# Kernel tuning notes

Hardware: AMD Instinct MI355X
Metric: run time of the kernel (lower is better)

The kernel has to match this reference:

```python
import jax, jax.numpy as jnp
import numpy as np

N = 100_000   # nodes
E = 1_600_000 # edges (avg degree 16)
D_IN = 128
D_H = 128
PROP_STEP = 2


def setup_inputs() -> dict:
    key = jax.random.key(0)
    k = jax.random.split(key, 6)
    in_feat = jax.random.normal(k[0], (N, D_IN), dtype=jnp.float32)
    edge_index = jax.random.randint(k[1], (2, E), 0, N, dtype=jnp.int64)
    s1 = 1.0 / np.sqrt(D_IN)
    s2 = 1.0 / np.sqrt(D_H)
    W1 = jax.random.normal(k[2], (D_IN, D_H), dtype=jnp.float32) * s1
    b1 = jnp.zeros((D_H,), dtype=jnp.float32)
    W2 = jax.random.normal(k[3], (D_H, D_H), dtype=jnp.float32) * s2
    b2 = jnp.zeros((D_H,), dtype=jnp.float32)
    return {"in_feat": in_feat, "edge_index": edge_index,
            "W1": W1, "b1": b1, "W2": W2, "b2": b2}


def _degree_norms(src, dst):
    ones = jnp.ones((src.shape[0],), dtype=jnp.float32)
    deg_out = jax.ops.segment_sum(ones, src, num_segments=N)
    deg_in = jax.ops.segment_sum(ones, dst, num_segments=N)
    # DGL clamps degree to >= 1 before norm='both'
    dout = jnp.maximum(deg_out, 1.0) ** -0.5  # applied to source features
    din = jnp.maximum(deg_in, 1.0) ** -0.5    # applied after aggregation
    return dout, din


def _gcn_conv(x, src, dst, dout, din, W, b):
    # D_in^{-1/2} A D_out^{-1/2} X W + b  (DGL GraphConv, norm='both')
    m = (x * dout[:, None])[src]                      # [E, D] gather
    agg = jax.ops.segment_sum(m, dst, num_segments=N) # [N, D] scatter-add
    return (agg * din[:, None]) @ W + b


def reference(in_feat, edge_index, W1, b1, W2, b2):
    src, dst = edge_index[0], edge_index[1]
    dout, din = _degree_norms(src, dst)
    h = _gcn_conv(in_feat, src, dst, dout, din, W1, b1)
    for _ in range(1, PROP_STEP):
        # relu=False and eval mode -> no relu / dropout
        h = _gcn_conv(h, src, dst, dout, din, W2, b2)
    return h
```

## Files before the change

### kernel.cpp

```cpp
#include <hip/hip_runtime.h>
#include <cstdint>
#include <cstddef>

#define DF 128
#define PB 512
#define RSH 8
#define RNG 256
#define CAP 6144

typedef short bf16x8 __attribute__((ext_vector_type(8)));
typedef float f32x4 __attribute__((ext_vector_type(4)));

__device__ __forceinline__ unsigned short f2b(float f) {
  unsigned u = __builtin_bit_cast(unsigned, f);
  u = (u + 0x7FFFu + ((u >> 16) & 1u)) >> 16;
  return (unsigned short)u;
}
__device__ __forceinline__ float b2f(unsigned short h) {
  return __builtin_bit_cast(float, (unsigned)h << 16);
}
__device__ __forceinline__ unsigned pack2(float lo, float hi) {
  return (unsigned)f2b(lo) | ((unsigned)f2b(hi) << 16);
}

__device__ __forceinline__ int edge_at(const void* ei, long long idx, int is32) {
  return is32 ? ((const int*)ei)[idx] : (int)((const long long*)ei)[idx];
}

__device__ __forceinline__ int detect_is32(const void* ei, long long lo, long long hi,
                                           int* s_flag) {
  int t = threadIdx.x;
  if (t == 0) *s_flag = 0;
  __syncthreads();
  int bad = 0;
  long long cap = lo + 2048; if (cap > hi) cap = hi;
  for (long long e = lo + t; e < cap; e += blockDim.x)
    bad |= (((const unsigned*)ei)[2 * e + 1] != 0);
  if (bad) atomicOr(s_flag, 1);
  __syncthreads();
  return *s_flag;
}

__global__ __launch_bounds__(256) void part_count_kernel(
    const void* __restrict__ ei, long long E, int nbuck, int chunk,
    int* __restrict__ H) {
  __shared__ int hd[512], hs[512], s_flag;
  int blk = blockIdx.x, t = threadIdx.x;
  for (int i = t; i < 512; i += 256) { hd[i] = 0; hs[i] = 0; }
  long long lo = (long long)blk * chunk;
  long long hi = lo + chunk; if (hi > E) hi = E;
  int is32 = detect_is32(ei, lo, hi, &s_flag);
  for (long long e = lo + t; e < hi; e += 256) {
    int s = edge_at(ei, e, is32);
    int d = edge_at(ei, E + e, is32);
    atomicAdd(&hs[s >> RSH], 1);
    atomicAdd(&hd[d >> RSH], 1);
  }
  __syncthreads();
  for (int b = t; b < nbuck; b += 256) {
    H[(size_t)b * PB + blk] = hd[b];
    H[((size_t)nbuck + b) * PB + blk] = hs[b];
  }
}

__device__ __forceinline__ int wave_incl_scan(int v, int lane) {
#pragma unroll
  for (int off = 1; off < 64; off <<= 1) {
    int t = __shfl_up(v, off, 64);
    if (lane >= off) v += t;
  }
  return v;
}

__global__ void chunk_sum_kernel(const int* __restrict__ deg, int* __restrict__ partials,
                                 int n, int nb,
                                 const float* __restrict__ W1, const float* __restrict__ W2,
                                 unsigned short* __restrict__ Wswz) {
  if ((int)blockIdx.x >= nb) {
    int chunk = ((int)blockIdx.x - nb) * 1024 + threadIdx.x;
    if (chunk < 8192) {
      int w = chunk >> 12;
      int rem = chunk & 4095;
      int part = rem >> 11;
      int tt = (rem >> 6) & 31;
      int l = rem & 63;
      int jb = tt >> 2, ks = tt & 3;
      const float* W = w ? W2 : W1;
      int c = jb * 16 + (l & 15);
      int k0 = ks * 32 + ((l >> 4) << 3);
      unsigned v[4];
#pragma unroll
      for (int p = 0; p < 4; ++p) {
        float f0 = W[(size_t)(k0 + 2 * p) * DF + c];
        float f1 = W[(size_t)(k0 + 2 * p + 1) * DF + c];
        unsigned short h0 = f2b(f0), h1 = f2b(f1);
        unsigned short o0 = part ? f2b(f0 - b2f(h0)) : h0;
        unsigned short o1 = part ? f2b(f1 - b2f(h1)) : h1;
        v[p] = (unsigned)o0 | ((unsigned)o1 << 16);
      }
      uint4 o; o.x = v[0]; o.y = v[1]; o.z = v[2]; o.w = v[3];
      ((uint4*)Wswz)[chunk] = o;
    }
    return;
  }
  __shared__ int wsum[16];
  int tid = threadIdx.x, lane = tid & 63, wid = tid >> 6;
  int base = blockIdx.x * 4096 + tid * 4;
  int s = 0;
#pragma unroll
  for (int q = 0; q < 4; ++q) { int i = base + q; if (i < n) s += deg[i]; }
#pragma unroll
  for (int off = 32; off; off >>= 1) s += __shfl_down(s, off, 64);
  if (lane == 0) wsum[wid] = s;
  __syncthreads();
  if (tid == 0) {
    int t = 0;
#pragma unroll
    for (int w = 0; w < 16; ++w) t += wsum[w];
    partials[blockIdx.x] = t;
  }
}

__global__ void scan_partials_kernel(int* __restrict__ partials, int nb) {
  int lane = threadIdx.x;
  int carry = 0;
  for (int base = 0; base < nb; base += 64) {
    int i = base + lane;
    int v = (i < nb) ? partials[i] : 0;
    int s = wave_incl_scan(v, lane);
    if (i < nb) partials[i] = s - v + carry;
    carry += __shfl(s, 63, 64);
  }
}

__global__ void scan_chunk_kernel(const int* __restrict__ deg, const int* __restrict__ chunk_off,
                                  int* __restrict__ row_ptr, int n) {
  __shared__ int wsum[16];
  int tid = threadIdx.x, lane = tid & 63, wid = tid >> 6;
  int base = blockIdx.x * 4096 + tid * 4;
  int v0 = (base + 0 < n) ? deg[base + 0] : 0;
  int v1 = (base + 1 < n) ? deg[base + 1] : 0;
  int v2 = (base + 2 < n) ? deg[base + 2] : 0;
  int v3 = (base + 3 < n) ? deg[base + 3] : 0;
  int p0 = v0, p1 = p0 + v1, p2 = p1 + v2, p3 = p2 + v3;
  int ws = wave_incl_scan(p3, lane);
  if (lane == 63) wsum[wid] = ws;
  __syncthreads();
  if (wid == 0) {
    int x = (lane < 16) ? wsum[lane] : 0;
    x = wave_incl_scan(x, lane);
    if (lane < 16) wsum[lane] = x;
  }
  __syncthreads();
  int off = (wid > 0 ? wsum[wid - 1] : 0) + (ws - p3) + chunk_off[blockIdx.x];
  if (base + 0 < n) row_ptr[base + 1] = off + p0;
  if (base + 1 < n) row_ptr[base + 2] = off + p1;
  if (base + 2 < n) row_ptr[base + 3] = off + p2;
  if (base + 3 < n) row_ptr[base + 4] = off + p3;
  if (blockIdx.x == 0 && tid == 0) row_ptr[0] = 0;
}

__global__ __launch_bounds__(256) void part_scatter_kernel(
    const void* __restrict__ ei, long long E, int nbuck, int chunk,
    const int* __restrict__ Hs, unsigned* __restrict__ pack_d,
    unsigned char* __restrict__ src_loc) {
  __shared__ int hd[512], hs[512], bd[512], bs[512];
  __shared__ int s_flag;
  int blk = blockIdx.x, t = threadIdx.x;
  for (int i = t; i < 512; i += 256) { hd[i] = 0; hs[i] = 0; }
  for (int b = t; b < nbuck; b += 256) {
    bd[b] = Hs[(size_t)b * PB + blk];
    bs[b] = Hs[((size_t)nbuck + b) * PB + blk] - (int)E;
  }
  long long lo = (long long)blk * chunk;
  long long hi = lo + chunk; if (hi > E) hi = E;
  int is32 = detect_is32(ei, lo, hi, &s_flag);
  for (long long e = lo + t; e < hi; e += 256) {
    int s = edge_at(ei, e, is32);
    int d = edge_at(ei, E + e, is32);
    int kb = d >> RSH;
    int rd = atomicAdd(&hd[kb], 1);
    pack_d[bd[kb] + rd] = ((unsigned)(d & (RNG - 1)) << 24) | (unsigned)s;
    int ks = s >> RSH;
    int rs = atomicAdd(&hs[ks], 1);
    src_loc[bs[ks] + rs] = (unsigned char)(s & (RNG - 1));
  }
}

__global__ __launch_bounds__(256) void bucket_build_kernel(
    const unsigned* __restrict__ pack_d, const unsigned char* __restrict__ src_loc,
    const int* __restrict__ Hs, int nbuck, long long E, int n,
    int* __restrict__ row_ptr, float* __restrict__ nin, float* __restrict__ nout,
    int* __restrict__ csr_src,
    const float* __restrict__ in_feat, unsigned short* __restrict__ x1h) {
  __shared__ unsigned stage[CAP];
  __shared__ int cnt[RNG], cur[RNG], woff[4];
  __shared__ float fn[RNG];
  int b = blockIdx.x, t = threadIdx.x;
  int lane = t & 63, wv = t >> 6;
  int start = Hs[(size_t)b * PB];
  int end = Hs[(size_t)(b + 1) * PB];
  int len = end - start;
  cnt[t] = 0;
  __syncthreads();
  bool fits = (len <= CAP);
  for (int i = t; i < len; i += 256) {
    unsigned p = pack_d[start + i];
    if (fits) stage[i] = p;
    atomicAdd(&cnt[p >> 24], 1);
  }
  __syncthreads();
  int dreg = cnt[t];
  int isc = wave_incl_scan(dreg, lane);
  if (lane == 63) woff[wv] = isc;
  __syncthreads();
  int add = 0;
#pragma unroll
  for (int w = 0; w < 4; ++w) if (w < wv) add += woff[w];
  int excl = isc - dreg + add;
  int nd = b * RNG + t;
  if (nd < n) {
    row_ptr[nd] = start + excl;
    nin[nd] = rsqrtf((float)(dreg > 1 ? dreg : 1));
  }
  if (b == (int)gridDim.x - 1 && t == 0) row_ptr[n] = (int)E;
  cur[t] = excl;
  __syncthreads();
  for (int i = t; i < len; i += 256) {
    unsigned p = fits ? stage[i] : pack_d[start + i];
    int dl = (int)(p >> 24);
    int r = atomicAdd(&cur[dl], 1);
    csr_src[start + r] = (int)(p & 0xFFFFFFu);
  }
  __syncthreads();
  cnt[t] = 0;
  __syncthreads();
  int sstart = Hs[(size_t)(nbuck + b) * PB] - (int)E;
  int send = Hs[(size_t)(nbuck + b + 1) * PB] - (int)E;
  for (int i = sstart + t; i < send; i += 256) atomicAdd(&cnt[src_loc[i]], 1);
  __syncthreads();
  float nv = rsqrtf((float)(cnt[t] > 1 ? cnt[t] : 1));
  fn[t] = nv;
  if (nd < n) nout[nd] = nv;
  __syncthreads();
  for (int c = t; c < RNG * DF / 8; c += 256) {
    int jl = c >> 4;
    int node = b * RNG + jl;
    if (node >= n) break;
    float s = fn[jl];
    long long base = (long long)node * DF + (c & 15) * 8;
    float4 a = *((const float4*)(in_feat + base));
    float4 bb = *((const float4*)(in_feat + base + 4));
    uint4 o;
    o.x = pack2(a.x * s, a.y * s);
    o.y = pack2(a.z * s, a.w * s);
    o.z = pack2(bb.x * s, bb.y * s);
    o.w = pack2(bb.z * s, bb.w * s);
    *((uint4*)(x1h + base)) = o;
  }
}

__global__ __launch_bounds__(256) void aggregate_bf16_kernel(
    const unsigned short* __restrict__ xh, const int* __restrict__ row_ptr,
    const int* __restrict__ csr_src, unsigned short* __restrict__ aggh, int n) {
  int wave = blockIdx.x * (blockDim.x >> 6) + (threadIdx.x >> 6);
  int lane = threadIdx.x & 63;
  if (wave >= n) return;
  int beg = row_ptr[wave], end = row_ptr[wave + 1];
  int deg = end - beg;
  int half = lane >> 5;
  int sub = lane & 31;
  float ax = 0.f, ay = 0.f, az = 0.f, aw = 0.f;
  for (int j0 = 0; j0 < deg; j0 += 64) {
    int li = beg + j0 + lane;
    int idx = csr_src[li < end ? li : (end - 1)];
    int cnt = deg - j0; if (cnt > 64) cnt = 64;
    int tfull = (cnt >> 4) << 3;
    for (int t0 = 0; t0 < tfull; t0 += 8) {
      ushort4 v[8];
#pragma unroll
      for (int u = 0; u < 8; ++u) {
        int s = __shfl(idx, 2 * (t0 + u) + half, 64);
        v[u] = *((const ushort4*)(xh + (size_t)s * DF) + sub);
      }
#pragma unroll
      for (int u = 0; u < 8; ++u) {
        ax += b2f(v[u].x); ay += b2f(v[u].y);
        az += b2f(v[u].z); aw += b2f(v[u].w);
      }
    }
    int cnt2 = (cnt + 1) >> 1;
    for (int t = tfull; t < cnt2; ++t) {
      int p = 2 * t + half;
      int s = __shfl(idx, p, 64);
      float m = (p < cnt) ? 1.f : 0.f;
      ushort4 v = *((const ushort4*)(xh + (size_t)s * DF) + sub);
      ax += b2f(v.x) * m; ay += b2f(v.y) * m;
      az += b2f(v.z) * m; aw += b2f(v.w) * m;
    }
  }
  ax += __shfl_down(ax, 32, 64);
  ay += __shfl_down(ay, 32, 64);
  az += __shfl_down(az, 32, 64);
  aw += __shfl_down(aw, 32, 64);
  if (half == 0) {
    uint2 pk; pk.x = pack2(ax, ay); pk.y = pack2(az, aw);
    *((uint2*)(aggh + (size_t)wave * DF + sub * 4)) = pk;
  }
}

template <int BF16OUT>
__global__ __launch_bounds__(256) void transform_mfma_kernel(
    const unsigned short* __restrict__ aggh, const unsigned short* __restrict__ Wswz,
    const float* __restrict__ nin, const float* __restrict__ bias,
    const float* __restrict__ sc_out, void* __restrict__ outp, int n, int ntiles) {
  __shared__ uint4 Wl[4096];
  __shared__ float ost[4][16 * 64];
  int tid = threadIdx.x;
  for (int i = tid; i < 4096; i += 256) Wl[i] = ((const uint4*)Wswz)[i];
  __syncthreads();
  int l = tid & 63, wv = tid >> 6;
  int lr = l & 15, lg = l >> 4;
  float* st = ost[wv];
  for (int tile = blockIdx.x; tile < ntiles; tile += gridDim.x) {
    int rowbase = tile * 64 + wv * 16;
    int r_eff = rowbase + lr; if (r_eff > n - 1) r_eff = n - 1;
    const unsigned short* arow = aggh + (size_t)r_eff * DF + (lg << 3);
    bf16x8 a0 = *(const bf16x8*)(arow);
    bf16x8 a1 = *(const bf16x8*)(arow + 32);
    bf16x8 a2 = *(const bf16x8*)(arow + 64);
    bf16x8 a3 = *(const bf16x8*)(arow + 96);
    f32x4 acc[8];
#pragma unroll
    for (int jb = 0; jb < 8; ++jb) acc[jb] = (f32x4){0.f, 0.f, 0.f, 0.f};
#pragma unroll
    for (int ks = 0; ks < 4; ++ks) {
      bf16x8 a = (ks == 0) ? a0 : (ks == 1) ? a1 : (ks == 2) ? a2 : a3;
#pragma unroll
      for (int jb = 0; jb < 8; ++jb) {
        bf16x8 bh = *(const bf16x8*)&Wl[(jb * 4 + ks) * 64 + l];
        acc[jb] = __builtin_amdgcn_mfma_f32_16x16x32_bf16(a, bh, acc[jb], 0, 0, 0);
        bf16x8 bl = *(const bf16x8*)&Wl[2048 + (jb * 4 + ks) * 64 + l];
        acc[jb] = __builtin_amdgcn_mfma_f32_16x16x32_bf16(a, bl, acc[jb], 0, 0, 0);
      }
    }
    float ninq[4], soq[4];
#pragma unroll
    for (int q = 0; q < 4; ++q) {
      int r = rowbase + lg * 4 + q;
      ninq[q] = (r < n) ? nin[r] : 0.f;
      soq[q] = (r < n) ? (sc_out ? sc_out[r] : 1.f) : 0.f;
    }
    int rmax = n - rowbase;
#pragma unroll
    for (int h = 0; h < 2; ++h) {
#pragma unroll
      for (int jb4 = 0; jb4 < 4; ++jb4) {
        int jb = h * 4 + jb4;
        float bj = bias[jb * 16 + lr];
#pragma unroll
        for (int q = 0; q < 4; ++q) {
          st[(lg * 4 + q) * 64 + jb4 * 16 + lr] = (acc[jb][q] * ninq[q] + bj) * soq[q];
        }
      }
      if (BF16OUT) {
#pragma unroll
        for (int it = 0; it < 2; ++it) {
          int id = it * 64 + l;
          int row = id >> 3, c8 = id & 7;
          if (row < rmax) {
            float4 va = *((const float4*)&st[row * 64 + c8 * 8]);
            float4 vb = *((const float4*)&st[row * 64 + c8 * 8 + 4]);
            uint4 o;
            o.x = pack2(va.x, va.y); o.y = pack2(va.z, va.w);
            o.z = pack2(vb.x, vb.y); o.w = pack2(vb.z, vb.w);
            *((uint4*)((unsigned short*)outp + (size_t)(rowbase + row) * DF + h * 64 + c8 * 8)) = o;
          }
        }
      } else {
#pragma unroll
        for (int it = 0; it < 4; ++it) {
          int id = it * 64 + l;
          int row = id >> 4, c4 = id & 15;
          if (row < rmax) {
            float4 v = *((const float4*)&st[row * 64 + c4 * 4]);
            *((float4*)((float*)outp + (size_t)(rowbase + row) * DF + h * 64 + c4 * 4)) = v;
          }
        }
      }
    }
  }
}

extern "C" void kernel_launch(void* const* d_in, const int* in_sizes, int n_in,
                              void* d_out, int out_size, void* d_ws, size_t ws_size,
                              hipStream_t stream) {
  const float* in_feat = (const float*)d_in[0];
  const void*  ei      = d_in[1];
  const float* W1 = (const float*)d_in[2];
  const float* b1 = (const float*)d_in[3];
  const float* W2 = (const float*)d_in[4];
  const float* b2 = (const float*)d_in[5];
  float* out = (float*)d_out;

  const int N = in_sizes[0] / DF;
  const long long E = in_sizes[1] / 2;
  const int nbuck = (N + RNG - 1) >> RSH;
  const int M = 2 * nbuck * PB;
  const int NB2 = (M + 4095) / 4096;
  const int chunk = (int)((E + PB - 1) / PB);
  const int ntiles = (N + 63) / 64;

  size_t off = 0;
  auto take = [&](size_t nb) -> char* {
    char* p = (char*)d_ws + off;
    off += (nb + 255) & ~(size_t)255;
    return p;
  };
  int* H          = (int*)take((size_t)M * 4);
  int* Hs         = (int*)take((size_t)(M + 1) * 4);
  int* partials   = (int*)take((size_t)NB2 * 4);
  int* row_ptr    = (int*)take((size_t)(N + 1) * 4);
  float* nout     = (float*)take((size_t)N * 4);
  float* nin      = (float*)take((size_t)N * 4);
  unsigned* pack_d = (unsigned*)take((size_t)E * 4);
  unsigned char* src_loc = (unsigned char*)take((size_t)E);
  int* csr_src    = (int*)take((size_t)E * 4);
  unsigned short* x1h = (unsigned short*)take((size_t)N * DF * 2);
  unsigned short* h1h = (unsigned short*)take((size_t)N * DF * 2);
  unsigned short* aggh = (unsigned short*)take((size_t)N * DF * 2);
  unsigned short* Wswz = (unsigned short*)take(2 * 65536);
  (void)ws_size; (void)n_in; (void)out_size;

  part_count_kernel<<<PB, 256, 0, stream>>>(ei, E, nbuck, chunk, H);
  chunk_sum_kernel<<<NB2 + 8, 1024, 0, stream>>>(H, partials, M, NB2, W1, W2, Wswz);
  scan_partials_kernel<<<1, 64, 0, stream>>>(partials, NB2);
  scan_chunk_kernel<<<NB2, 1024, 0, stream>>>(H, partials, Hs, M);
  part_scatter_kernel<<<PB, 256, 0, stream>>>(ei, E, nbuck, chunk, Hs, pack_d, src_loc);
  bucket_build_kernel<<<nbuck, 256, 0, stream>>>(pack_d, src_loc, Hs, nbuck, E, N,
                                                 row_ptr, nin, nout, csr_src,
                                                 in_feat, x1h);

  int ab = (N + 3) / 4;
  aggregate_bf16_kernel<<<ab, 256, 0, stream>>>(x1h, row_ptr, csr_src, aggh, N);
  transform_mfma_kernel<1><<<512, 256, 0, stream>>>(aggh, Wswz, nin, b1, nout, h1h, N, ntiles);
  aggregate_bf16_kernel<<<ab, 256, 0, stream>>>(h1h, row_ptr, csr_src, aggh, N);
  transform_mfma_kernel<0><<<512, 256, 0, stream>>>(aggh, Wswz + 32768, nin, b2, nullptr, out, N, ntiles);
}
```

Measured before the change: 261.4 us.

## Replace three-kernel scan with decoupled lookback scan; double rows per MFMA tile

The separate chunk-sum, partial-scan and chunk-scan kernels over the bucket histogram are merged into one single-pass scan that uses decoupled lookback through a descriptor array cleared by a memset. This removes two kernel launches and a serial pass over the partials. The MFMA transform kernel now handles 128 rows per tile, with two row sets per wave sharing each loaded weight fragment, and bias is hoisted out of the tile loop. Risks are spin-waiting on block order for lookback correctness and higher register pressure in the transform.

Result: no change. 266.2 us (+1.8%).

```diff
diff --git a/kernel.cpp b/kernel.cpp
--- a/kernel.cpp
+++ b/kernel.cpp
@@ -7,6 +7,7 @@
 #define RSH 8
 #define RNG 256
 #define CAP 6144
+#define SCH 4096
 
 typedef short bf16x8 __attribute__((ext_vector_type(8)));
 typedef float f32x4 __attribute__((ext_vector_type(4)));
@@ -72,12 +73,13 @@
   return v;
 }
 
-__global__ void chunk_sum_kernel(const int* __restrict__ deg, int* __restrict__ partials,
-                                 int n, int nb,
-                                 const float* __restrict__ W1, const float* __restrict__ W2,
-                                 unsigned short* __restrict__ Wswz) {
-  if ((int)blockIdx.x >= nb) {
-    int chunk = ((int)blockIdx.x - nb) * 1024 + threadIdx.x;
+__global__ __launch_bounds__(1024) void scan_lookback_kernel(
+    const int* __restrict__ H, int* __restrict__ Hs, unsigned* __restrict__ desc,
+    int m, int nblk,
+    const float* __restrict__ W1, const float* __restrict__ W2,
+    unsigned short* __restrict__ Wswz) {
+  if ((int)blockIdx.x >= nblk) {
+    int chunk = ((int)blockIdx.x - nblk) * 1024 + threadIdx.x;
     if (chunk < 8192) {
       int w = chunk >> 12;
       int rem = chunk & 4095;
@@ -104,44 +106,13 @@
     return;
   }
   __shared__ int wsum[16];
+  __shared__ int s_excl;
   int tid = threadIdx.x, lane = tid & 63, wid = tid >> 6;
-  int base = blockIdx.x * 4096 + tid * 4;
-  int s = 0;
-#pragma unroll
-  for (int q = 0; q < 4; ++q) { int i = base + q; if (i < n) s += deg[i]; }
-#pragma unroll
-  for (int off = 32; off; off >>= 1) s += __shfl_down(s, off, 64);
-  if (lane == 0) wsum[wid] = s;
-  __syncthreads();
-  if (tid == 0) {
-    int t = 0;
-#pragma unroll
-    for (int w = 0; w < 16; ++w) t += wsum[w];
-    partials[blockIdx.x] = t;
-  }
-}
-
-__global__ void scan_partials_kernel(int* __restrict__ partials, int nb) {
-  int lane = threadIdx.x;
-  int carry = 0;
-  for (int base = 0; base < nb; base += 64) {
-    int i = base + lane;
-    int v = (i < nb) ? partials[i] : 0;
-    int s = wave_incl_scan(v, lane);
-    if (i < nb) partials[i] = s - v + carry;
-    carry += __shfl(s, 63, 64);
-  }
-}
-
-__global__ void scan_chunk_kernel(const int* __restrict__ deg, const int* __restrict__ chunk_off,
-                                  int* __restrict__ row_ptr, int n) {
-  __shared__ int wsum[16];
-  int tid = threadIdx.x, lane = tid & 63, wid = tid >> 6;
-  int base = blockIdx.x * 4096 + tid * 4;
-  int v0 = (base + 0 < n) ? deg[base + 0] : 0;
-  int v1 = (base + 1 < n) ? deg[base + 1] : 0;
-  int v2 = (base + 2 < n) ? deg[base + 2] : 0;
-  int v3 = (base + 3 < n) ? deg[base + 3] : 0;
+  int base = blockIdx.x * SCH + tid * 4;
+  int v0 = (base + 0 < m) ? H[base + 0] : 0;
+  int v1 = (base + 1 < m) ? H[base + 1] : 0;
+  int v2 = (base + 2 < m) ? H[base + 2] : 0;
+  int v3 = (base + 3 < m) ? H[base + 3] : 0;
   int p0 = v0, p1 = p0 + v1, p2 = p1 + v2, p3 = p2 + v3;
   int ws = wave_incl_scan(p3, lane);
   if (lane == 63) wsum[wid] = ws;
@@ -152,12 +123,35 @@
     if (lane < 16) wsum[lane] = x;
   }
   __syncthreads();
-  int off = (wid > 0 ? wsum[wid - 1] : 0) + (ws - p3) + chunk_off[blockIdx.x];
-  if (base + 0 < n) row_ptr[base + 1] = off + p0;
-  if (base + 1 < n) row_ptr[base + 2] = off + p1;
-  if (base + 2 < n) row_ptr[base + 3] = off + p2;
-  if (base + 3 < n) row_ptr[base + 4] = off + p3;
-  if (blockIdx.x == 0 && tid == 0) row_ptr[0] = 0;
+  if (tid == 0) {
+    int S = wsum[15];
+    if (blockIdx.x == 0) {
+      __hip_atomic_store(&desc[0], ((unsigned)S << 2) | 2u,
+                         __ATOMIC_RELEASE, __HIP_MEMORY_SCOPE_AGENT);
+      s_excl = 0;
+    } else {
+      __hip_atomic_store(&desc[blockIdx.x], ((unsigned)S << 2) | 1u,
+                         __ATOMIC_RELEASE, __HIP_MEMORY_SCOPE_AGENT);
+      unsigned ex = 0;
+      int j = (int)blockIdx.x - 1;
+      for (;;) {
+        unsigned d = __hip_atomic_load(&desc[j], __ATOMIC_ACQUIRE, __HIP_MEMORY_SCOPE_AGENT);
+        unsigned stt = d & 3u;
+        if (stt == 2u) { ex += (d >> 2); break; }
+        if (stt == 1u) { ex += (d >> 2); --j; }
+      }
+      __hip_atomic_store(&desc[blockIdx.x], (((unsigned)S + ex) << 2) | 2u,
+                         __ATOMIC_RELEASE, __HIP_MEMORY_SCOPE_AGENT);
+      s_excl = (int)ex;
+    }
+  }
+  __syncthreads();
+  int off = (wid > 0 ? wsum[wid - 1] : 0) + (ws - p3) + s_excl;
+  if (base + 0 < m) Hs[base + 1] = off + p0;
+  if (base + 1 < m) Hs[base + 2] = off + p1;
+  if (base + 2 < m) Hs[base + 3] = off + p2;
+  if (base + 3 < m) Hs[base + 4] = off + p3;
+  if (blockIdx.x == 0 && tid == 0) Hs[0] = 0;
 }
 
 __global__ __launch_bounds__(256) void part_scatter_kernel(
@@ -322,69 +316,84 @@
   int l = tid & 63, wv = tid >> 6;
   int lr = l & 15, lg = l >> 4;
   float* st = ost[wv];
+  float bj[8];
+#pragma unroll
+  for (int jb = 0; jb < 8; ++jb) bj[jb] = bias[jb * 16 + lr];
   for (int tile = blockIdx.x; tile < ntiles; tile += gridDim.x) {
-    int rowbase = tile * 64 + wv * 16;
-    int r_eff = rowbase + lr; if (r_eff > n - 1) r_eff = n - 1;
-    const unsigned short* arow = aggh + (size_t)r_eff * DF + (lg << 3);
-    bf16x8 a0 = *(const bf16x8*)(arow);
-    bf16x8 a1 = *(const bf16x8*)(arow + 32);
-    bf16x8 a2 = *(const bf16x8*)(arow + 64);
-    bf16x8 a3 = *(const bf16x8*)(arow + 96);
-    f32x4 acc[8];
-#pragma unroll
-    for (int jb = 0; jb < 8; ++jb) acc[jb] = (f32x4){0.f, 0.f, 0.f, 0.f};
+    int rb0 = tile * 128 + wv * 16;
+    int rb1 = rb0 + 64;
+    bf16x8 a[2][4];
+#pragma unroll
+    for (int s = 0; s < 2; ++s) {
+      int r_eff = (s ? rb1 : rb0) + lr; if (r_eff > n - 1) r_eff = n - 1;
+      const unsigned short* arow = aggh + (size_t)r_eff * DF + (lg << 3);
+      a[s][0] = *(const bf16x8*)(arow);
+      a[s][1] = *(const bf16x8*)(arow + 32);
+      a[s][2] = *(const bf16x8*)(arow + 64);
+      a[s][3] = *(const bf16x8*)(arow + 96);
+    }
+    f32x4 acc[2][8];
+#pragma unroll
+    for (int s = 0; s < 2; ++s)
+#pragma unroll
+      for (int jb = 0; jb < 8; ++jb) acc[s][jb] = (f32x4){0.f, 0.f, 0.f, 0.f};
 #pragma unroll
     for (int ks = 0; ks < 4; ++ks) {
-      bf16x8 a = (ks == 0) ? a0 : (ks == 1) ? a1 : (ks == 2) ? a2 : a3;
 #pragma unroll
       for (int jb = 0; jb < 8; ++jb) {
         bf16x8 bh = *(const bf16x8*)&Wl[(jb * 4 + ks) * 64 + l];
-        acc[jb] = __builtin_amdgcn_mfma_f32_16x16x32_bf16(a, bh, acc[jb], 0, 0, 0);
         bf16x8 bl = *(const bf16x8*)&Wl[2048 + (jb * 4 + ks) * 64 + l];
-        acc[jb] = __builtin_amdgcn_mfma_f32_16x16x32_bf16(a, bl, acc[jb], 0, 0, 0);
-      }
-    }
-    float ninq[4], soq[4];
-#pragma unroll
-    for (int q = 0; q < 4; ++q) {
-      int r = rowbase + lg * 4 + q;
-      ninq[q] = (r < n) ? nin[r] : 0.f;
-      soq[q] = (r < n) ? (sc_out ? sc_out[r] : 1.f) : 0.f;
-    }
-    int rmax = n - rowbase;
-#pragma unroll
-    for (int h = 0; h < 2; ++h) {
-#pragma unroll
-      for (int jb4 = 0; jb4 < 4; ++jb4) {
-        int jb = h * 4 + jb4;
-        float bj = bias[jb * 16 + lr];
-#pragma unroll
-        for (int q = 0; q < 4; ++q) {
-          st[(lg * 4 + q) * 64 + jb4 * 16 + lr] = (acc[jb][q] * ninq[q] + bj) * soq[q];
-        }
-      }
-      if (BF16OUT) {
-#pragma unroll
-        for (int it = 0; it < 2; ++it) {
-          int id = it * 64 + l;
-          int row = id >> 3, c8 = id & 7;
-          if (row < rmax) {
-            float4 va = *((const float4*)&st[row * 64 + c8 * 8]);
-            float4 vb = *((const float4*)&st[row * 64 + c8 * 8 + 4]);
-            uint4 o;
-            o.x = pack2(va.x, va.y); o.y = pack2(va.z, va.w);
-            o.z = pack2(vb.x, vb.y); o.w = pack2(vb.z, vb.w);
-            *((uint4*)((unsigned short*)outp + (size_t)(rowbase + row) * DF + h * 64 + c8 * 8)) = o;
+        acc[0][jb] = __builtin_amdgcn_mfma_f32_16x16x32_bf16(a[0][ks], bh, acc[0][jb], 0, 0, 0);
+        acc[0][jb] = __builtin_amdgcn_mfma_f32_16x16x32_bf16(a[0][ks], bl, acc[0][jb], 0, 0, 0);
+        acc[1][jb] = __builtin_amdgcn_mfma_f32_16x16x32_bf16(a[1][ks], bh, acc[1][jb], 0, 0, 0);
+        acc[1][jb] = __builtin_amdgcn_mfma_f32_16x16x32_bf16(a[1][ks], bl, acc[1][jb], 0, 0, 0);
+      }
+    }
+#pragma unroll
+    for (int s = 0; s < 2; ++s) {
+      int rowbase = s ? rb1 : rb0;
+      float ninq[4], soq[4];
+#pragma unroll
+      for (int q = 0; q < 4; ++q) {
+        int r = rowbase + lg * 4 + q;
+        ninq[q] = (r < n) ? nin[r] : 0.f;
+        soq[q] = (r < n) ? (sc_out ? sc_out[r] : 1.f) : 0.f;
+      }
+      int rmax = n - rowbase;
+#pragma unroll
+      for (int h = 0; h < 2; ++h) {
+#pragma unroll
+        for (int jb4 = 0; jb4 < 4; ++jb4) {
+          int jb = h * 4 + jb4;
+#pragma unroll
+          for (int q = 0; q < 4; ++q) {
+            st[(lg * 4 + q) * 64 + jb4 * 16 + lr] =
+                (acc[s][jb][q] * ninq[q] + bj[jb]) * soq[q];
           }
         }
-      } else {
-#pragma unroll
-        for (int it = 0; it < 4; ++it) {
-          int id = it * 64 + l;
-          int row = id >> 4, c4 = id & 15;
-          if (row < rmax) {
-            float4 v = *((const float4*)&st[row * 64 + c4 * 4]);
-            *((float4*)((float*)outp + (size_t)(rowbase + row) * DF + h * 64 + c4 * 4)) = v;
+        if (BF16OUT) {
+#pragma unroll
+          for (int it = 0; it < 2; ++it) {
+            int id = it * 64 + l;
+            int row = id >> 3, c8 = id & 7;
+            if (row < rmax) {
+              float4 va = *((const float4*)&st[row * 64 + c8 * 8]);
+              float4 vb = *((const float4*)&st[row * 64 + c8 * 8 + 4]);
+              uint4 o;
+              o.x = pack2(va.x, va.y); o.y = pack2(va.z, va.w);
+              o.z = pack2(vb.x, vb.y); o.w = pack2(vb.z, vb.w);
+              *((uint4*)((unsigned short*)outp + (size_t)(rowbase + row) * DF + h * 64 + c8 * 8)) = o;
+            }
+          }
+        } else {
+#pragma unroll
+          for (int it = 0; it < 4; ++it) {
+            int id = it * 64 + l;
+            int row = id >> 4, c4 = id & 15;
+            if (row < rmax) {
+              float4 v = *((const float4*)&st[row * 64 + c4 * 4]);
+              *((float4*)((float*)outp + (size_t)(rowbase + row) * DF + h * 64 + c4 * 4)) = v;
+            }
           }
         }
       }
@@ -407,9 +416,9 @@
   const long long E = in_sizes[1] / 2;
   const int nbuck = (N + RNG - 1) >> RSH;
   const int M = 2 * nbuck * PB;
-  const int NB2 = (M + 4095) / 4096;
+  const int NBLK = (M + SCH - 1) / SCH;
   const int chunk = (int)((E + PB - 1) / PB);
-  const int ntiles = (N + 63) / 64;
+  const int ntiles = (N + 127) / 128;
 
   size_t off = 0;
   auto take = [&](size_t nb) -> char* {
@@ -419,7 +428,7 @@
   };
   int* H          = (int*)take((size_t)M * 4);
   int* Hs         = (int*)take((size_t)(M + 1) * 4);
-  int* partials   = (int*)take((size_t)NB2 * 4);
+  unsigned* desc  = (unsigned*)take((size_t)NBLK * 4);
   int* row_ptr    = (int*)take((size_t)(N + 1) * 4);
   float* nout     = (float*)take((size_t)N * 4);
   float* nin      = (float*)take((size_t)N * 4);
@@ -432,10 +441,9 @@
   unsigned short* Wswz = (unsigned short*)take(2 * 65536);
   (void)ws_size; (void)n_in; (void)out_size;
 
+  hipMemsetAsync(desc, 0, (size_t)NBLK * 4, stream);
   part_count_kernel<<<PB, 256, 0, stream>>>(ei, E, nbuck, chunk, H);
-  chunk_sum_kernel<<<NB2 + 8, 1024, 0, stream>>>(H, partials, M, NB2, W1, W2, Wswz);
-  scan_partials_kernel<<<1, 64, 0, stream>>>(partials, NB2);
-  scan_chunk_kernel<<<NB2, 1024, 0, stream>>>(H, partials, Hs, M);
+  scan_lookback_kernel<<<NBLK + 8, 1024, 0, stream>>>(H, Hs, desc, M, NBLK, W1, W2, Wswz);
   part_scatter_kernel<<<PB, 256, 0, stream>>>(ei, E, nbuck, chunk, Hs, pack_d, src_loc);
   bucket_build_kernel<<<nbuck, 256, 0, stream>>>(pack_d, src_loc, Hs, nbuck, E, N,
                                                  row_ptr, nin, nout, csr_src,
```
